# Performance work log

Hardware: AMD Instinct MI355X
Metric: run time of the kernel (lower is better)

## Reference

```python
import jax, jax.numpy as jnp
import numpy as np

NUM_NODES = 100000
NUM_EDGES = 3200000
NUM_GRAPHS = 512
IN_DIM, OUT_DIM = 128, 16
DIMS = [IN_DIM, 32, 48, 64]


def glorot(key, shape):
    lim = float(np.sqrt(6.0 / (shape[0] + shape[1])))
    return jax.random.uniform(key, shape, jnp.float32, -lim, lim)


def setup_inputs() -> dict:
    key = jax.random.key(0)
    ks = jax.random.split(key, 12)
    x = jax.random.normal(ks[0], (NUM_NODES, IN_DIM), jnp.float32)
    edge_index = jax.random.randint(ks[1], (2, NUM_EDGES), 0, NUM_NODES, jnp.int64)
    batch = jnp.sort(jax.random.randint(ks[2], (NUM_NODES,), 0, NUM_GRAPHS, jnp.int64))
    params = {}
    for i in range(3):
        params[f"W{i+1}"] = glorot(ks[3 + i], (DIMS[i], DIMS[i + 1]))
        params[f"b{i+1}"] = jnp.zeros((DIMS[i + 1],), jnp.float32)
    params["fc1_w"] = glorot(ks[6], (64, 32))
    params["fc1_b"] = jnp.zeros((32,), jnp.float32)
    params["fc2_w"] = glorot(ks[7], (32, OUT_DIM))
    params["fc2_b"] = jnp.zeros((OUT_DIM,), jnp.float32)
    return {"x": x, "edge_index": edge_index, "batch": batch, **params}


def gcn_conv(x, W, b, src, dst, deg_inv_sqrt):
    # h = x @ W; aggregate with symmetric normalization + self loops (PyG GCNConv)
    h = x @ W  # [N, out]
    norm = deg_inv_sqrt[src] * deg_inv_sqrt[dst]  # [E]
    msg = h[src] * norm[:, None]  # [E, out]  (gather)
    agg = jnp.zeros_like(h).at[dst].add(msg)  # scatter-add to targets
    self_loop = h * (deg_inv_sqrt * deg_inv_sqrt)[:, None]
    return agg + self_loop + b


def reference(x, edge_index, batch, W1, b1, W2, b2, W3, b3, fc1_w, fc1_b, fc2_w, fc2_b):
    src, dst = edge_index[0], edge_index[1]
    n = x.shape[0]
    # degree with self loops: deg[i] = in-degree + 1
    deg = jnp.zeros((n,), jnp.float32).at[dst].add(1.0) + 1.0
    dis = jax.lax.rsqrt(deg)
    h = jax.nn.relu(gcn_conv(x, W1, b1, src, dst, dis))
    h = jax.nn.relu(gcn_conv(h, W2, b2, src, dst, dis))
    h = jax.nn.relu(gcn_conv(h, W3, b3, src, dst, dis))
    # global mean pool per graph
    sums = jax.ops.segment_sum(h, batch, num_segments=NUM_GRAPHS)
    cnts = jax.ops.segment_sum(jnp.ones((n,), jnp.float32), batch, num_segments=NUM_GRAPHS)
    pooled = sums / jnp.maximum(cnts, 1.0)[:, None]  # [G, 64]
    z = jax.nn.relu(pooled @ fc1_w + fc1_b)
    logits = z @ fc2_w + fc2_b
    return jax.nn.softmax(logits, axis=1)
```

## Files before the change

kernel.cpp:

```cpp
#include <hip/hip_runtime.h>
#include <hip/hip_fp16.h>

static constexpr int NN = 100000;
static constexpr int NE = 3200000;
static constexpr int NG = 512;
static constexpr int NCB = 196;
static constexpr int CHK = 8192;
static constexpr int NCH = (NE + CHK - 1) / CHK;
static constexpr int NCNT = NCB * NCH;
static constexpr int SCAN_BLK = 2048;
static constexpr int NSB = (NCNT + SCAN_BLK - 1) / SCAN_BLK;

typedef float f32x2 __attribute__((ext_vector_type(2)));

__device__ __forceinline__ void acc_fp8x4(unsigned v, float* a) {
    f32x2 lo = __builtin_amdgcn_cvt_pk_f32_fp8((int)v, false);
    f32x2 hi = __builtin_amdgcn_cvt_pk_f32_fp8((int)v, true);
    a[0] += lo.x; a[1] += lo.y; a[2] += hi.x; a[3] += hi.y;
}
__device__ __forceinline__ void set_fp8x4(unsigned v, float* a) {
    f32x2 lo = __builtin_amdgcn_cvt_pk_f32_fp8((int)v, false);
    f32x2 hi = __builtin_amdgcn_cvt_pk_f32_fp8((int)v, true);
    a[0] = lo.x; a[1] = lo.y; a[2] = hi.x; a[3] = hi.y;
}
__device__ __forceinline__ unsigned pack_fp8x4(float a, float b, float c, float d) {
    int p = __builtin_amdgcn_cvt_pk_fp8_f32(a, b, 0, false);
    p = __builtin_amdgcn_cvt_pk_fp8_f32(c, d, p, true);
    return (unsigned)p;
}

__global__ __launch_bounds__(256) void k_histC(const int* __restrict__ dst,
                                               int* __restrict__ cntC, int e) {
    __shared__ int h[NCB];
    for (int i = threadIdx.x; i < NCB; i += 256) h[i] = 0;
    __syncthreads();
    const int s = blockIdx.x * CHK, eend = min(s + CHK, e);
    for (int i = s + threadIdx.x; i < eend; i += 256)
        atomicAdd(&h[dst[i] >> 9], 1);
    __syncthreads();
    for (int i = threadIdx.x; i < NCB; i += 256)
        cntC[(size_t)i * NCH + blockIdx.x] = h[i];
}

__global__ __launch_bounds__(256) void k_scanA(const int* __restrict__ in,
                                               int* __restrict__ out,
                                               int* __restrict__ bsum, int n) {
    __shared__ int s[256];
    const int tid = threadIdx.x;
    const int base = blockIdx.x * SCAN_BLK + tid * 8;
    int v[8], t = 0;
#pragma unroll
    for (int c = 0; c < 8; c++) {
        int idx = base + c;
        v[c] = (idx < n) ? in[idx] : 0;
        t += v[c];
    }
    s[tid] = t;
    __syncthreads();
    for (int off = 1; off < 256; off <<= 1) {
        int x = (tid >= off) ? s[tid - off] : 0;
        __syncthreads();
        s[tid] += x;
        __syncthreads();
    }
    if (tid == 255) bsum[blockIdx.x] = s[255];
    int run = s[tid] - t;
#pragma unroll
    for (int c = 0; c < 8; c++) {
        int idx = base + c;
        if (idx < n) out[idx] = run;
        run += v[c];
    }
}

__global__ __launch_bounds__(256) void k_scanB(int* __restrict__ bsum, int nb) {
    __shared__ int s[256];
    const int tid = threadIdx.x;
    int v = (tid < nb) ? bsum[tid] : 0;
    s[tid] = v;
    __syncthreads();
    for (int off = 1; off < 256; off <<= 1) {
        int x = (tid >= off) ? s[tid - off] : 0;
        __syncthreads();
        s[tid] += x;
        __syncthreads();
    }
    if (tid < nb) bsum[tid] = s[tid] - v;
}

__global__ __launch_bounds__(256) void k_scanC(int* __restrict__ out,
                                               const int* __restrict__ bsum, int n) {
    int i = blockIdx.x * 256 + threadIdx.x;
    if (i < n) out[i] += bsum[i / SCAN_BLK];
}

__global__ __launch_bounds__(256) void k_scatC(const int* __restrict__ src,
                                               const int* __restrict__ dst,
                                               const int* __restrict__ scC,
                                               unsigned* __restrict__ tmp, int e) {
    __shared__ int cur[NCB];
    for (int i = threadIdx.x; i < NCB; i += 256)
        cur[i] = scC[(size_t)i * NCH + blockIdx.x];
    __syncthreads();
    const int s = blockIdx.x * CHK, eend = min(s + CHK, e);
    for (int i = s + threadIdx.x; i < eend; i += 256) {
        int d = dst[i];
        int p = atomicAdd(&cur[d >> 9], 1);
        tmp[p] = ((unsigned)(d & 511) << 17) | (unsigned)src[i];
    }
}

__global__ __launch_bounds__(1024) void k_fill512(const unsigned* __restrict__ tmp,
                                                  const int* __restrict__ scC,
                                                  int* __restrict__ csr,
                                                  int* __restrict__ degi,
                                                  int* __restrict__ offs,
                                                  float* __restrict__ dis,
                                                  int n, int etotal) {
    __shared__ int cnt[512];
    __shared__ int s[512];
    __shared__ int cur[512];
    const int b = blockIdx.x, tid = threadIdx.x;
    if (tid < 512) cnt[tid] = 0;
    const int e0 = scC[(size_t)b * NCH];
    const int e1 = (b + 1 < NCB) ? scC[(size_t)(b + 1) * NCH] : etotal;
    __syncthreads();
    for (int e = e0 + tid; e < e1; e += 1024)
        atomicAdd(&cnt[tmp[e] >> 17], 1);
    __syncthreads();
    int v = 0;
    if (tid < 512) { v = cnt[tid]; s[tid] = v; }
    __syncthreads();
    for (int off = 1; off < 512; off <<= 1) {
        int x = 0;
        if (tid < 512 && tid >= off) x = s[tid - off];
        __syncthreads();
        if (tid < 512) s[tid] += x;
        __syncthreads();
    }
    if (tid < 512) {
        int c = e0 + s[tid] - v;
        cur[tid] = c;
        int node = b * 512 + tid;
        if (node < n) {
            degi[node] = v;
            offs[node] = c;
            dis[node] = rsqrtf((float)v + 1.0f);
        }
    }
    __syncthreads();
    for (int e = e0 + tid; e < e1; e += 1024) {
        unsigned pk = tmp[e];
        int p = atomicAdd(&cur[pk >> 17], 1);
        csr[p] = (int)(pk & 0x1FFFFu);
    }
}

__global__ __launch_bounds__(256) void k_gemm1(const float* __restrict__ X,
                                               const float* __restrict__ W,
                                               const float* __restrict__ dis,
                                               unsigned* __restrict__ H, int n) {
    constexpr int IN = 128, ROWS = 32;
    __shared__ float sW[IN * 32];
    __shared__ float sX[ROWS][IN];
    const int tid = threadIdx.x;
    for (int i = tid; i < IN * 32; i += 256) sW[i] = W[i];
    const int row0 = blockIdx.x * ROWS;
    const float4* X4 = (const float4*)X;
    for (int i = tid; i < ROWS * 32; i += 256) {
        int r = row0 + (i >> 5);
        float4 v = make_float4(0.f, 0.f, 0.f, 0.f);
        if (r < n) v = X4[(size_t)r * 32 + (i & 31)];
        ((float4*)&sX[i >> 5][0])[i & 31] = v;
    }
    __syncthreads();
    const int lr = tid >> 3;
    const int cg = tid & 7;
    const int gr = row0 + lr;
    float acc[4] = {0.f, 0.f, 0.f, 0.f};
#pragma unroll 8
    for (int k = 0; k < IN; k++) {
        float xv = sX[lr][k];
#pragma unroll
        for (int c = 0; c < 4; c++)
            acc[c] = fmaf(xv, sW[k * 32 + 4 * cg + c], acc[c]);
    }
    if (gr < n) {
        float dd = dis[gr];
        H[(size_t)gr * 8 + cg] =
            pack_fp8x4(acc[0] * dd, acc[1] * dd, acc[2] * dd, acc[3] * dd);
    }
}

__global__ __launch_bounds__(256) void k_pull2(
        const unsigned* __restrict__ Hp, const int* __restrict__ offs,
        const int* __restrict__ degi, const int* __restrict__ csr,
        const float* __restrict__ dis, const float* __restrict__ b,
        unsigned* __restrict__ A, int n) {
    const int group = threadIdx.x >> 3, j0 = threadIdx.x & 7;
    const int d = blockIdx.x * 32 + group;
    if (d >= n) return;
    float acc[4];
    set_fp8x4(Hp[(size_t)d * 8 + j0], acc);
    int e = offs[d];
    const int end = e + degi[d];
    for (; e + 7 < end; e += 8) {
        unsigned v0 = Hp[(size_t)csr[e] * 8 + j0];
        unsigned v1 = Hp[(size_t)csr[e + 1] * 8 + j0];
        unsigned v2 = Hp[(size_t)csr[e + 2] * 8 + j0];
        unsigned v3 = Hp[(size_t)csr[e + 3] * 8 + j0];
        unsigned v4 = Hp[(size_t)csr[e + 4] * 8 + j0];
        unsigned v5 = Hp[(size_t)csr[e + 5] * 8 + j0];
        unsigned v6 = Hp[(size_t)csr[e + 6] * 8 + j0];
        unsigned v7 = Hp[(size_t)csr[e + 7] * 8 + j0];
        acc_fp8x4(v0, acc); acc_fp8x4(v1, acc);
        acc_fp8x4(v2, acc); acc_fp8x4(v3, acc);
        acc_fp8x4(v4, acc); acc_fp8x4(v5, acc);
        acc_fp8x4(v6, acc); acc_fp8x4(v7, acc);
    }
    for (; e < end; e++) acc_fp8x4(Hp[(size_t)csr[e] * 8 + j0], acc);
    const float dd = dis[d];
    float r[4];
#pragma unroll
    for (int c = 0; c < 4; c++)
        r[c] = fmaxf(fmaf(acc[c], dd, b[4 * j0 + c]), 0.f) * dd;
    A[(size_t)d * 8 + j0] = pack_fp8x4(r[0], r[1], r[2], r[3]);
}

__global__ __launch_bounds__(256) void k_pullmm32(
        const unsigned* __restrict__ Hp, const int* __restrict__ offs,
        const int* __restrict__ degi, const int* __restrict__ csr,
        const float* __restrict__ dis, const float* __restrict__ W,
        const float* __restrict__ b, unsigned* __restrict__ A, int n) {
    __shared__ float sW[32 * 48];
    __shared__ float rows[32][32];
    __shared__ float aout[32][48];
    for (int i = threadIdx.x; i < 32 * 48; i += 256) sW[i] = W[i];
    const int group = threadIdx.x >> 3, j0 = threadIdx.x & 7;
    const int d = blockIdx.x * 32 + group;
    if (d < n) {
        float acc[4];
        set_fp8x4(Hp[(size_t)d * 8 + j0], acc);
        int e = offs[d];
        const int end = e + degi[d];
        for (; e + 7 < end; e += 8) {
            unsigned v0 = Hp[(size_t)csr[e] * 8 + j0];
            unsigned v1 = Hp[(size_t)csr[e + 1] * 8 + j0];
            unsigned v2 = Hp[(size_t)csr[e + 2] * 8 + j0];
            unsigned v3 = Hp[(size_t)csr[e + 3] * 8 + j0];
            unsigned v4 = Hp[(size_t)csr[e + 4] * 8 + j0];
            unsigned v5 = Hp[(size_t)csr[e + 5] * 8 + j0];
            unsigned v6 = Hp[(size_t)csr[e + 6] * 8 + j0];
            unsigned v7 = Hp[(size_t)csr[e + 7] * 8 + j0];
            acc_fp8x4(v0, acc); acc_fp8x4(v1, acc);
            acc_fp8x4(v2, acc); acc_fp8x4(v3, acc);
            acc_fp8x4(v4, acc); acc_fp8x4(v5, acc);
            acc_fp8x4(v6, acc); acc_fp8x4(v7, acc);
        }
        for (; e < end; e++) acc_fp8x4(Hp[(size_t)csr[e] * 8 + j0], acc);
        const float dd = dis[d];
#pragma unroll
        for (int c = 0; c < 4; c++) rows[group][4 * j0 + c] = acc[c] * dd;
    }
    __syncthreads();
    const int row0 = blockIdx.x * 32;
#pragma unroll
    for (int o = 0; o < 6; o++) {
        int idx = o * 256 + threadIdx.x;
        int nl = idx / 48, col = idx % 48;
        float s = b[col];
#pragma unroll
        for (int k = 0; k < 32; k++)
            s = fmaf(rows[nl][k], sW[k * 48 + col], s);
        aout[nl][col] = fmaxf(s, 0.f) * dis[min(row0 + nl, n - 1)];
    }
    __syncthreads();
    for (int idx = threadIdx.x; idx < 32 * 16; idx += 256) {
        int nl = idx >> 4, cg = idx & 15;
        int gr = row0 + nl;
        if (gr < n) {
            unsigned p = 0;
            if (cg < 12)
                p = pack_fp8x4(aout[nl][4 * cg], aout[nl][4 * cg + 1],
                               aout[nl][4 * cg + 2], aout[nl][4 * cg + 3]);
            A[(size_t)gr * 16 + cg] = p;
        }
    }
}

__global__ __launch_bounds__(256) void k_pullmm48(
        const uint2* __restrict__ Hp, const int* __restrict__ offs,
        const int* __restrict__ degi, const int* __restrict__ csr,
        const float* __restrict__ dis, const float* __restrict__ W,
        const float* __restrict__ b, __half* __restrict__ A, int n) {
    __shared__ float sW[48 * 64];
    __shared__ float rows[32][48];
    for (int i = threadIdx.x; i < 48 * 64; i += 256) sW[i] = W[i];
    const int group = threadIdx.x >> 3, j0 = threadIdx.x & 7;
    const int d = blockIdx.x * 32 + group;
    if (d < n) {
        float acc[8];
        uint2 sv = Hp[(size_t)d * 8 + j0];
        set_fp8x4(sv.x, acc); set_fp8x4(sv.y, acc + 4);
        int e = offs[d];
        const int end = e + degi[d];
        for (; e + 7 < end; e += 8) {
            uint2 v0 = Hp[(size_t)csr[e] * 8 + j0];
            uint2 v1 = Hp[(size_t)csr[e + 1] * 8 + j0];
            uint2 v2 = Hp[(size_t)csr[e + 2] * 8 + j0];
            uint2 v3 = Hp[(size_t)csr[e + 3] * 8 + j0];
            uint2 v4 = Hp[(size_t)csr[e + 4] * 8 + j0];
            uint2 v5 = Hp[(size_t)csr[e + 5] * 8 + j0];
            uint2 v6 = Hp[(size_t)csr[e + 6] * 8 + j0];
            uint2 v7 = Hp[(size_t)csr[e + 7] * 8 + j0];
            acc_fp8x4(v0.x, acc); acc_fp8x4(v0.y, acc + 4);
            acc_fp8x4(v1.x, acc); acc_fp8x4(v1.y, acc + 4);
            acc_fp8x4(v2.x, acc); acc_fp8x4(v2.y, acc + 4);
            acc_fp8x4(v3.x, acc); acc_fp8x4(v3.y, acc + 4);
            acc_fp8x4(v4.x, acc); acc_fp8x4(v4.y, acc + 4);
            acc_fp8x4(v5.x, acc); acc_fp8x4(v5.y, acc + 4);
            acc_fp8x4(v6.x, acc); acc_fp8x4(v6.y, acc + 4);
            acc_fp8x4(v7.x, acc); acc_fp8x4(v7.y, acc + 4);
        }
        for (; e < end; e++) {
            uint2 v = Hp[(size_t)csr[e] * 8 + j0];
            acc_fp8x4(v.x, acc); acc_fp8x4(v.y, acc + 4);
        }
        const float dd = dis[d];
        if (j0 < 6) {
#pragma unroll
            for (int c = 0; c < 8; c++) rows[group][8 * j0 + c] = acc[c] * dd;
        }
    }
    __syncthreads();
    const int row0 = blockIdx.x * 32;
#pragma unroll
    for (int o = 0; o < 8; o++) {
        int idx = o * 256 + threadIdx.x;
        int nl = idx >> 6, col = idx & 63;
        int gr = row0 + nl;
        if (gr < n) {
            float s = b[col];
#pragma unroll
            for (int k = 0; k < 48; k++)
                s = fmaf(rows[nl][k], sW[k * 64 + col], s);
            A[(size_t)gr * 64 + col] = __float2half(s);
        }
    }
}

__global__ __launch_bounds__(256) void k_bounds(const int* __restrict__ batch,
                                                int* __restrict__ bounds,
                                                int n, int ngr) {
    int g = blockIdx.x * 256 + threadIdx.x;
    if (g > ngr) return;
    if (g == ngr) { bounds[g] = n; return; }
    int lo = 0, hi = n;
    while (lo < hi) {
        int mid = (lo + hi) >> 1;
        if (batch[mid] < g) lo = mid + 1; else hi = mid;
    }
    bounds[g] = lo;
}

__global__ __launch_bounds__(256) void k_pool(const __half* __restrict__ A3,
                                              const int* __restrict__ bounds,
                                              float* __restrict__ pooled) {
    const int g = blockIdx.x;
    const int j = threadIdx.x & 63, rl = threadIdx.x >> 6;
    const int s = bounds[g], e = bounds[g + 1];
    float sum = 0.f;
    for (int node = s + rl; node < e; node += 4)
        sum += fmaxf(__half2float(A3[(size_t)node * 64 + j]), 0.f);
    __shared__ float red[4][64];
    red[rl][j] = sum;
    __syncthreads();
    if (rl == 0)
        pooled[g * 64 + j] = (red[0][j] + red[1][j] + red[2][j] + red[3][j]) /
                             fmaxf((float)(e - s), 1.f);
}

__global__ __launch_bounds__(64) void k_head(
        const float* __restrict__ pooled,
        const float* __restrict__ f1w, const float* __restrict__ f1b,
        const float* __restrict__ f2w, const float* __restrict__ f2b,
        float* __restrict__ out) {
    int g = blockIdx.x;
    int t = threadIdx.x;
    __shared__ float p[64], z[32], lg[16];
    p[t] = pooled[g * 64 + t];
    __syncthreads();
    if (t < 32) {
        float acc = f1b[t];
        for (int j = 0; j < 64; j++) acc = fmaf(p[j], f1w[j * 32 + t], acc);
        z[t] = fmaxf(acc, 0.f);
    }
    __syncthreads();
    if (t < 16) {
        float acc = f2b[t];
        for (int k = 0; k < 32; k++) acc = fmaf(z[k], f2w[k * 16 + t], acc);
        lg[t] = acc;
    }
    __syncthreads();
    if (t < 16) {
        float m = lg[0];
        for (int i = 1; i < 16; i++) m = fmaxf(m, lg[i]);
        float s = 0.f;
        for (int i = 0; i < 16; i++) s += expf(lg[i] - m);
        out[g * 16 + t] = expf(lg[t] - m) / s;
    }
}

extern "C" void kernel_launch(void* const* d_in, const int* in_sizes, int n_in,
                              void* d_out, int out_size, void* d_ws, size_t ws_size,
                              hipStream_t stream) {
    (void)in_sizes; (void)n_in; (void)out_size; (void)ws_size;
    const float* x     = (const float*)d_in[0];
    const int*   ei    = (const int*)d_in[1];
    const int*   batch = (const int*)d_in[2];
    const float* W1 = (const float*)d_in[3];
    const float* b1 = (const float*)d_in[4];
    const float* W2 = (const float*)d_in[5];  const float* b2 = (const float*)d_in[6];
    const float* W3 = (const float*)d_in[7];  const float* b3 = (const float*)d_in[8];
    const float* f1w = (const float*)d_in[9]; const float* f1b = (const float*)d_in[10];
    const float* f2w = (const float*)d_in[11];const float* f2b = (const float*)d_in[12];
    float* out = (float*)d_out;

    const int* src = ei;
    const int* dst = ei + NE;

    float* ws = (float*)d_ws;
    size_t o = 0;
    float* dis    = ws + o; o += NN;
    int*   degi   = (int*)(ws + o); o += NN;
    int*   offs   = (int*)(ws + o); o += NN;
    int*   cntC   = (int*)(ws + o); o += 76640;
    int*   scC    = (int*)(ws + o); o += 76640;
    int*   bsum   = (int*)(ws + o); o += 48;
    int*   bounds = (int*)(ws + o); o += 528;
    float* pooled = ws + o; o += (size_t)NG * 64;
    int*   csr    = (int*)(ws + o); o += NE;
    unsigned* TA  = (unsigned*)(ws + o); o += NE;
    unsigned* H1  = (unsigned*)(ws + o); o += NN * 8;
    unsigned* H2  = (unsigned*)(ws + o); o += NN * 8;
    unsigned* H3  = (unsigned*)(ws + o); o += NN * 16;

    unsigned* tmp = TA;
    __half*   A3  = (__half*)TA;

    k_histC<<<NCH, 256, 0, stream>>>(dst, cntC, NE);
    k_scanA<<<NSB, 256, 0, stream>>>(cntC, scC, bsum, NCNT);
    k_scanB<<<1, 256, 0, stream>>>(bsum, NSB);
    k_scanC<<<(NCNT + 255) / 256, 256, 0, stream>>>(scC, bsum, NCNT);
    k_scatC<<<NCH, 256, 0, stream>>>(src, dst, scC, tmp, NE);
    k_fill512<<<NCB, 1024, 0, stream>>>(tmp, scC, csr, degi, offs, dis, NN, NE);

    const int PGRID = (NN + 31) / 32;

    k_gemm1<<<(NN + 31) / 32, 256, 0, stream>>>(x, W1, dis, H1, NN);
    k_pull2<<<PGRID, 256, 0, stream>>>(H1, offs, degi, csr, dis, b1, H2, NN);

    k_pullmm32<<<PGRID, 256, 0, stream>>>(H2, offs, degi, csr, dis, W2, b2, H3, NN);

    k_pullmm48<<<PGRID, 256, 0, stream>>>(
        (const uint2*)H3, offs, degi, csr, dis, W3, b3, A3, NN);

    k_bounds<<<(NG + 1 + 255) / 256, 256, 0, stream>>>(batch, bounds, NN, NG);
    k_pool<<<NG, 256, 0, stream>>>(A3, bounds, pooled);
    k_head<<<NG, 64, 0, stream>>>(pooled, f1w, f1b, f2w, f2b, out);
}
```

Measured before the change: 387.1 us.

## Fold scan fixup into consumers, fuse pool/head, nontemporal csr loads

```diff
diff --git a/kernel.cpp b/kernel.cpp
--- a/kernel.cpp
+++ b/kernel.cpp
@@ -88,19 +88,16 @@
     if (tid < nb) bsum[tid] = s[tid] - v;
 }
 
-__global__ __launch_bounds__(256) void k_scanC(int* __restrict__ out,
-                                               const int* __restrict__ bsum, int n) {
-    int i = blockIdx.x * 256 + threadIdx.x;
-    if (i < n) out[i] += bsum[i / SCAN_BLK];
-}
-
 __global__ __launch_bounds__(256) void k_scatC(const int* __restrict__ src,
                                                const int* __restrict__ dst,
-                                               const int* __restrict__ scC,
+                                               const int* __restrict__ sc,
+                                               const int* __restrict__ bsum,
                                                unsigned* __restrict__ tmp, int e) {
     __shared__ int cur[NCB];
-    for (int i = threadIdx.x; i < NCB; i += 256)
-        cur[i] = scC[(size_t)i * NCH + blockIdx.x];
+    for (int i = threadIdx.x; i < NCB; i += 256) {
+        size_t idx = (size_t)i * NCH + blockIdx.x;
+        cur[i] = sc[idx] + bsum[idx >> 11];
+    }
     __syncthreads();
     const int s = blockIdx.x * CHK, eend = min(s + CHK, e);
     for (int i = s + threadIdx.x; i < eend; i += 256) {
@@ -111,7 +108,8 @@
 }
 
 __global__ __launch_bounds__(1024) void k_fill512(const unsigned* __restrict__ tmp,
-                                                  const int* __restrict__ scC,
+                                                  const int* __restrict__ sc,
+                                                  const int* __restrict__ bsum,
                                                   int* __restrict__ csr,
                                                   int* __restrict__ degi,
                                                   int* __restrict__ offs,
@@ -122,8 +120,13 @@
     __shared__ int cur[512];
     const int b = blockIdx.x, tid = threadIdx.x;
     if (tid < 512) cnt[tid] = 0;
-    const int e0 = scC[(size_t)b * NCH];
-    const int e1 = (b + 1 < NCB) ? scC[(size_t)(b + 1) * NCH] : etotal;
+    size_t i0 = (size_t)b * NCH;
+    const int e0 = sc[i0] + bsum[i0 >> 11];
+    int e1 = etotal;
+    if (b + 1 < NCB) {
+        size_t i1 = (size_t)(b + 1) * NCH;
+        e1 = sc[i1] + bsum[i1 >> 11];
+    }
     __syncthreads();
     for (int e = e0 + tid; e < e1; e += 1024)
         atomicAdd(&cnt[tmp[e] >> 17], 1);
@@ -205,20 +208,21 @@
     int e = offs[d];
     const int end = e + degi[d];
     for (; e + 7 < end; e += 8) {
-        unsigned v0 = Hp[(size_t)csr[e] * 8 + j0];
-        unsigned v1 = Hp[(size_t)csr[e + 1] * 8 + j0];
-        unsigned v2 = Hp[(size_t)csr[e + 2] * 8 + j0];
-        unsigned v3 = Hp[(size_t)csr[e + 3] * 8 + j0];
-        unsigned v4 = Hp[(size_t)csr[e + 4] * 8 + j0];
-        unsigned v5 = Hp[(size_t)csr[e + 5] * 8 + j0];
-        unsigned v6 = Hp[(size_t)csr[e + 6] * 8 + j0];
-        unsigned v7 = Hp[(size_t)csr[e + 7] * 8 + j0];
+        unsigned v0 = Hp[(size_t)__builtin_nontemporal_load(csr + e) * 8 + j0];
+        unsigned v1 = Hp[(size_t)__builtin_nontemporal_load(csr + e + 1) * 8 + j0];
+        unsigned v2 = Hp[(size_t)__builtin_nontemporal_load(csr + e + 2) * 8 + j0];
+        unsigned v3 = Hp[(size_t)__builtin_nontemporal_load(csr + e + 3) * 8 + j0];
+        unsigned v4 = Hp[(size_t)__builtin_nontemporal_load(csr + e + 4) * 8 + j0];
+        unsigned v5 = Hp[(size_t)__builtin_nontemporal_load(csr + e + 5) * 8 + j0];
+        unsigned v6 = Hp[(size_t)__builtin_nontemporal_load(csr + e + 6) * 8 + j0];
+        unsigned v7 = Hp[(size_t)__builtin_nontemporal_load(csr + e + 7) * 8 + j0];
         acc_fp8x4(v0, acc); acc_fp8x4(v1, acc);
         acc_fp8x4(v2, acc); acc_fp8x4(v3, acc);
         acc_fp8x4(v4, acc); acc_fp8x4(v5, acc);
         acc_fp8x4(v6, acc); acc_fp8x4(v7, acc);
     }
-    for (; e < end; e++) acc_fp8x4(Hp[(size_t)csr[e] * 8 + j0], acc);
+    for (; e < end; e++)
+        acc_fp8x4(Hp[(size_t)__builtin_nontemporal_load(csr + e) * 8 + j0], acc);
     const float dd = dis[d];
     float r[4];
 #pragma unroll
@@ -233,8 +237,7 @@
         const float* __restrict__ dis, const float* __restrict__ W,
         const float* __restrict__ b, unsigned* __restrict__ A, int n) {
     __shared__ float sW[32 * 48];
-    __shared__ float rows[32][32];
-    __shared__ float aout[32][48];
+    __shared__ float rows[32][33];
     for (int i = threadIdx.x; i < 32 * 48; i += 256) sW[i] = W[i];
     const int group = threadIdx.x >> 3, j0 = threadIdx.x & 7;
     const int d = blockIdx.x * 32 + group;
@@ -244,45 +247,45 @@
         int e = offs[d];
         const int end = e + degi[d];
         for (; e + 7 < end; e += 8) {
-            unsigned v0 = Hp[(size_t)csr[e] * 8 + j0];
-            unsigned v1 = Hp[(size_t)csr[e + 1] * 8 + j0];
-            unsigned v2 = Hp[(size_t)csr[e + 2] * 8 + j0];
-            unsigned v3 = Hp[(size_t)csr[e + 3] * 8 + j0];
-            unsigned v4 = Hp[(size_t)csr[e + 4] * 8 + j0];
-            unsigned v5 = Hp[(size_t)csr[e + 5] * 8 + j0];
-            unsigned v6 = Hp[(size_t)csr[e + 6] * 8 + j0];
-            unsigned v7 = Hp[(size_t)csr[e + 7] * 8 + j0];
+            unsigned v0 = Hp[(size_t)__builtin_nontemporal_load(csr + e) * 8 + j0];
+            unsigned v1 = Hp[(size_t)__builtin_nontemporal_load(csr + e + 1) * 8 + j0];
+            unsigned v2 = Hp[(size_t)__builtin_nontemporal_load(csr + e + 2) * 8 + j0];
+            unsigned v3 = Hp[(size_t)__builtin_nontemporal_load(csr + e + 3) * 8 + j0];
+            unsigned v4 = Hp[(size_t)__builtin_nontemporal_load(csr + e + 4) * 8 + j0];
+            unsigned v5 = Hp[(size_t)__builtin_nontemporal_load(csr + e + 5) * 8 + j0];
+            unsigned v6 = Hp[(size_t)__builtin_nontemporal_load(csr + e + 6) * 8 + j0];
+            unsigned v7 = Hp[(size_t)__builtin_nontemporal_load(csr + e + 7) * 8 + j0];
             acc_fp8x4(v0, acc); acc_fp8x4(v1, acc);
             acc_fp8x4(v2, acc); acc_fp8x4(v3, acc);
             acc_fp8x4(v4, acc); acc_fp8x4(v5, acc);
             acc_fp8x4(v6, acc); acc_fp8x4(v7, acc);
         }
-        for (; e < end; e++) acc_fp8x4(Hp[(size_t)csr[e] * 8 + j0], acc);
+        for (; e < end; e++)
+            acc_fp8x4(Hp[(size_t)__builtin_nontemporal_load(csr + e) * 8 + j0], acc);
         const float dd = dis[d];
 #pragma unroll
         for (int c = 0; c < 4; c++) rows[group][4 * j0 + c] = acc[c] * dd;
     }
     __syncthreads();
     const int row0 = blockIdx.x * 32;
-#pragma unroll
-    for (int o = 0; o < 6; o++) {
-        int idx = o * 256 + threadIdx.x;
-        int nl = idx / 48, col = idx % 48;
-        float s = b[col];
-#pragma unroll
-        for (int k = 0; k < 32; k++)
-            s = fmaf(rows[nl][k], sW[k * 48 + col], s);
-        aout[nl][col] = fmaxf(s, 0.f) * dis[min(row0 + nl, n - 1)];
-    }
-    __syncthreads();
-    for (int idx = threadIdx.x; idx < 32 * 16; idx += 256) {
-        int nl = idx >> 4, cg = idx & 15;
+    for (int u = threadIdx.x; u < 32 * 16; u += 256) {
+        int nl = u >> 4, cg = u & 15;
         int gr = row0 + nl;
         if (gr < n) {
             unsigned p = 0;
-            if (cg < 12)
-                p = pack_fp8x4(aout[nl][4 * cg], aout[nl][4 * cg + 1],
-                               aout[nl][4 * cg + 2], aout[nl][4 * cg + 3]);
+            if (cg < 12) {
+                float dd2 = dis[gr];
+                float r[4];
+#pragma unroll
+                for (int c = 0; c < 4; c++) {
+                    float s = b[4 * cg + c];
+#pragma unroll
+                    for (int k = 0; k < 32; k++)
+                        s = fmaf(rows[nl][k], sW[k * 48 + 4 * cg + c], s);
+                    r[c] = fmaxf(s, 0.f) * dd2;
+                }
+                p = pack_fp8x4(r[0], r[1], r[2], r[3]);
+            }
             A[(size_t)gr * 16 + cg] = p;
         }
     }
@@ -294,7 +297,7 @@
         const float* __restrict__ dis, const float* __restrict__ W,
         const float* __restrict__ b, __half* __restrict__ A, int n) {
     __shared__ float sW[48 * 64];
-    __shared__ float rows[32][48];
+    __shared__ float rows[32][50];
     for (int i = threadIdx.x; i < 48 * 64; i += 256) sW[i] = W[i];
     const int group = threadIdx.x >> 3, j0 = threadIdx.x & 7;
     const int d = blockIdx.x * 32 + group;
@@ -305,14 +308,14 @@
         int e = offs[d];
         const int end = e + degi[d];
         for (; e + 7 < end; e += 8) {
-            uint2 v0 = Hp[(size_t)csr[e] * 8 + j0];
-            uint2 v1 = Hp[(size_t)csr[e + 1] * 8 + j0];
-            uint2 v2 = Hp[(size_t)csr[e + 2] * 8 + j0];
-            uint2 v3 = Hp[(size_t)csr[e + 3] * 8 + j0];
-            uint2 v4 = Hp[(size_t)csr[e + 4] * 8 + j0];
-            uint2 v5 = Hp[(size_t)csr[e + 5] * 8 + j0];
-            uint2 v6 = Hp[(size_t)csr[e + 6] * 8 + j0];
-            uint2 v7 = Hp[(size_t)csr[e + 7] * 8 + j0];
+            uint2 v0 = Hp[(size_t)__builtin_nontemporal_load(csr + e) * 8 + j0];
+            uint2 v1 = Hp[(size_t)__builtin_nontemporal_load(csr + e + 1) * 8 + j0];
+            uint2 v2 = Hp[(size_t)__builtin_nontemporal_load(csr + e + 2) * 8 + j0];
+            uint2 v3 = Hp[(size_t)__builtin_nontemporal_load(csr + e + 3) * 8 + j0];
+            uint2 v4 = Hp[(size_t)__builtin_nontemporal_load(csr + e + 4) * 8 + j0];
+            uint2 v5 = Hp[(size_t)__builtin_nontemporal_load(csr + e + 5) * 8 + j0];
+            uint2 v6 = Hp[(size_t)__builtin_nontemporal_load(csr + e + 6) * 8 + j0];
+            uint2 v7 = Hp[(size_t)__builtin_nontemporal_load(csr + e + 7) * 8 + j0];
             acc_fp8x4(v0.x, acc); acc_fp8x4(v0.y, acc + 4);
             acc_fp8x4(v1.x, acc); acc_fp8x4(v1.y, acc + 4);
             acc_fp8x4(v2.x, acc); acc_fp8x4(v2.y, acc + 4);
@@ -323,7 +326,7 @@
             acc_fp8x4(v7.x, acc); acc_fp8x4(v7.y, acc + 4);
         }
         for (; e < end; e++) {
-            uint2 v = Hp[(size_t)csr[e] * 8 + j0];
+            uint2 v = Hp[(size_t)__builtin_nontemporal_load(csr + e) * 8 + j0];
             acc_fp8x4(v.x, acc); acc_fp8x4(v.y, acc + 4);
         }
         const float dd = dis[d];
@@ -349,50 +352,40 @@
     }
 }
 
-__global__ __launch_bounds__(256) void k_bounds(const int* __restrict__ batch,
-                                                int* __restrict__ bounds,
-                                                int n, int ngr) {
-    int g = blockIdx.x * 256 + threadIdx.x;
-    if (g > ngr) return;
-    if (g == ngr) { bounds[g] = n; return; }
-    int lo = 0, hi = n;
-    while (lo < hi) {
-        int mid = (lo + hi) >> 1;
-        if (batch[mid] < g) lo = mid + 1; else hi = mid;
-    }
-    bounds[g] = lo;
-}
-
-__global__ __launch_bounds__(256) void k_pool(const __half* __restrict__ A3,
-                                              const int* __restrict__ bounds,
-                                              float* __restrict__ pooled) {
+__global__ __launch_bounds__(256) void k_poolhead(
+        const __half* __restrict__ A3, const int* __restrict__ batch,
+        const float* __restrict__ f1w, const float* __restrict__ f1b,
+        const float* __restrict__ f2w, const float* __restrict__ f2b,
+        float* __restrict__ out, int n, int ngr) {
     const int g = blockIdx.x;
+    __shared__ int sb[2];
+    if (threadIdx.x < 2) {
+        int target = g + threadIdx.x;
+        int lo = 0, hi = n;
+        while (lo < hi) {
+            int mid = (lo + hi) >> 1;
+            if (batch[mid] < target) lo = mid + 1; else hi = mid;
+        }
+        sb[threadIdx.x] = lo;
+    }
+    __syncthreads();
+    const int s = sb[0], e = sb[1];
     const int j = threadIdx.x & 63, rl = threadIdx.x >> 6;
-    const int s = bounds[g], e = bounds[g + 1];
     float sum = 0.f;
     for (int node = s + rl; node < e; node += 4)
         sum += fmaxf(__half2float(A3[(size_t)node * 64 + j]), 0.f);
     __shared__ float red[4][64];
+    __shared__ float p[64], z[32], lg[16];
     red[rl][j] = sum;
     __syncthreads();
     if (rl == 0)
-        pooled[g * 64 + j] = (red[0][j] + red[1][j] + red[2][j] + red[3][j]) /
-                             fmaxf((float)(e - s), 1.f);
-}
-
-__global__ __launch_bounds__(64) void k_head(
-        const float* __restrict__ pooled,
-        const float* __restrict__ f1w, const float* __restrict__ f1b,
-        const float* __restrict__ f2w, const float* __restrict__ f2b,
-        float* __restrict__ out) {
-    int g = blockIdx.x;
-    int t = threadIdx.x;
-    __shared__ float p[64], z[32], lg[16];
-    p[t] = pooled[g * 64 + t];
-    __syncthreads();
+        p[j] = (red[0][j] + red[1][j] + red[2][j] + red[3][j]) /
+               fmaxf((float)(e - s), 1.f);
+    __syncthreads();
+    const int t = threadIdx.x;
     if (t < 32) {
         float acc = f1b[t];
-        for (int j = 0; j < 64; j++) acc = fmaf(p[j], f1w[j * 32 + t], acc);
+        for (int k = 0; k < 64; k++) acc = fmaf(p[k], f1w[k * 32 + t], acc);
         z[t] = fmaxf(acc, 0.f);
     }
     __syncthreads();
@@ -405,9 +398,9 @@
     if (t < 16) {
         float m = lg[0];
         for (int i = 1; i < 16; i++) m = fmaxf(m, lg[i]);
-        float s = 0.f;
-        for (int i = 0; i < 16; i++) s += expf(lg[i] - m);
-        out[g * 16 + t] = expf(lg[t] - m) / s;
+        float sden = 0.f;
+        for (int i = 0; i < 16; i++) sden += expf(lg[i] - m);
+        out[g * 16 + t] = expf(lg[t] - m) / sden;
     }
 }
 
@@ -435,10 +428,8 @@
     int*   degi   = (int*)(ws + o); o += NN;
     int*   offs   = (int*)(ws + o); o += NN;
     int*   cntC   = (int*)(ws + o); o += 76640;
-    int*   scC    = (int*)(ws + o); o += 76640;
+    int*   sc     = (int*)(ws + o); o += 76640;
     int*   bsum   = (int*)(ws + o); o += 48;
-    int*   bounds = (int*)(ws + o); o += 528;
-    float* pooled = ws + o; o += (size_t)NG * 64;
     int*   csr    = (int*)(ws + o); o += NE;
     unsigned* TA  = (unsigned*)(ws + o); o += NE;
     unsigned* H1  = (unsigned*)(ws + o); o += NN * 8;
@@ -449,11 +440,10 @@
     __half*   A3  = (__half*)TA;
 
     k_histC<<<NCH, 256, 0, stream>>>(dst, cntC, NE);
-    k_scanA<<<NSB, 256, 0, stream>>>(cntC, scC, bsum, NCNT);
+    k_scanA<<<NSB, 256, 0, stream>>>(cntC, sc, bsum, NCNT);
     k_scanB<<<1, 256, 0, stream>>>(bsum, NSB);
-    k_scanC<<<(NCNT + 255) / 256, 256, 0, stream>>>(scC, bsum, NCNT);
-    k_scatC<<<NCH, 256, 0, stream>>>(src, dst, scC, tmp, NE);
-    k_fill512<<<NCB, 1024, 0, stream>>>(tmp, scC, csr, degi, offs, dis, NN, NE);
+    k_scatC<<<NCH, 256, 0, stream>>>(src, dst, sc, bsum, tmp, NE);
+    k_fill512<<<NCB, 1024, 0, stream>>>(tmp, sc, bsum, csr, degi, offs, dis, NN, NE);
 
     const int PGRID = (NN + 31) / 32;
 
@@ -465,7 +455,5 @@
     k_pullmm48<<<PGRID, 256, 0, stream>>>(
         (const uint2*)H3, offs, degi, csr, dis, W3, b3, A3, NN);
 
-    k_bounds<<<(NG + 1 + 255) / 256, 256, 0, stream>>>(batch, bounds, NN, NG);
-    k_pool<<<NG, 256, 0, stream>>>(A3, bounds, pooled);
-    k_head<<<NG, 64, 0, stream>>>(pooled, f1w, f1b, f2w, f2b, out);
-}
+    k_poolhead<<<NG, 256, 0, stream>>>(A3, batch, f1w, f1b, f2w, f2b, out, NN, NG);
+}
```

Measured after the change: 395.7 us. 1.02x slower.
